# Kernel optimization log

Hardware: AMD Instinct MI355X
Metric: run time of the kernel (lower is better)

The kernel has to match this reference:

```python
import jax, jax.numpy as jnp
import numpy as np

EPS_LN = 1e-5


def _ln(x, g, b):
    m = jnp.mean(x, axis=-1, keepdims=True)
    v = jnp.var(x, axis=-1, keepdims=True)
    return (x - m) * jax.lax.rsqrt(v + EPS_LN) * g + b


def setup_inputs() -> dict:
    B, T, D, DV, NV, DS = 8, 2048, 128, 32, 64, 16
    key = jax.random.key(0)
    ks = jax.random.split(key, 24)
    s = 0.02
    inp = {
        'x_head': jax.random.normal(ks[0], (B, T, D), jnp.float32),
        'gate': jax.random.uniform(ks[1], (B, T, 1), jnp.float32),
        'mask': jnp.zeros((1, T, T), jnp.float32),
        'node_bias_6d': jax.random.normal(ks[2], (6,), jnp.float32),
        'vertex_emb': jax.random.normal(ks[3], (NV, DV), jnp.float32),
        'adj_bias': jax.random.normal(ks[4], (NV, NV), jnp.float32),
        'spectral_emb': jax.random.normal(ks[5], (NV, DS), jnp.float32),
        'fractal_W_spec_weight': jax.random.normal(ks[6], (DV, DS), jnp.float32),
        # learned params (torch Linear weight is [out, in])
        'cn_g': jnp.ones((D,), jnp.float32), 'cn_b': jnp.zeros((D,), jnp.float32),
        'Wq': jax.random.normal(ks[7], (D, D), jnp.float32) * s,
        'Wk': jax.random.normal(ks[8], (D, D), jnp.float32) * s,
        'Wv': jax.random.normal(ks[9], (D, D), jnp.float32) * s,
        'bn_g': jnp.ones((D,), jnp.float32), 'bn_b': jnp.zeros((D,), jnp.float32),
        'Wg_w': jax.random.normal(ks[10], (6, D), jnp.float32) * s,
        'Wg_b': jnp.zeros((6,), jnp.float32),
        'g2v': jax.random.normal(ks[11], (DV, 6), jnp.float32) * s,
        'v2h': jax.random.normal(ks[12], (D, DV), jnp.float32) * s,
        'pc_w': jax.random.normal(ks[13], (D, 2 * D), jnp.float32) * s,
        'pc_b': jnp.zeros((D,), jnp.float32),
        'pn_g': jnp.ones((D,), jnp.float32), 'pn_b': jnp.zeros((D,), jnp.float32),
        'pu_w': jax.random.normal(ks[14], (2 * D, D), jnp.float32) * s,
        'pu_b': jnp.zeros((2 * D,), jnp.float32),
        'pd_w': jax.random.normal(ks[15], (D, 2 * D), jnp.float32) * s,
        'pd_b': jnp.zeros((D,), jnp.float32),
    }
    return inp


def reference(x_head, gate, mask, node_bias_6d, vertex_emb, adj_bias, spectral_emb,
              fractal_W_spec_weight, cn_g, cn_b, Wq, Wk, Wv, bn_g, bn_b, Wg_w, Wg_b,
              g2v, v2h, pc_w, pc_b, pn_g, pn_b, pu_w, pu_b, pd_w, pd_b):
    d_head = x_head.shape[-1]
    scale = jnp.asarray(np.sqrt(d_head), jnp.float32)

    # --- center: gated attention (scores in fp32) ---
    h = _ln(x_head, cn_g, cn_b)
    Q = (h @ Wq.T) * gate
    K = (h @ Wk.T) * gate
    V = h @ Wv.T
    scores = jnp.einsum('btd,bsd->bts', Q.astype(jnp.float32), K.astype(jnp.float32)) / scale
    scores = scores + mask
    alignment = scores  # head_index == 0
    attn = jax.nn.softmax(scores, axis=-1).astype(x_head.dtype)
    center_out = jnp.einsum('bts,bsd->btd', attn, V)
    center_signal = x_head + center_out

    # --- boundary: hypercube vertex routing with top-8 straight-through ---
    h_b = _ln(x_head, bn_g, bn_b)
    gates_6d = jax.nn.sigmoid(h_b @ Wg_w.T + Wg_b + node_bias_6d)      # [B,T,6]
    gate_proj = gates_6d @ g2v.T                                       # [B,T,DV]
    v_scores = gate_proj @ vertex_emb.T                                # [B,T,NV]
    spec_proj = spectral_emb @ fractal_W_spec_weight.T                 # [NV,DV]
    v_scores = v_scores + 0.1 * (gate_proj @ spec_proj.T)
    v_scores = v_scores + 0.1 * (v_scores @ adj_bias)

    mean_abs = jax.lax.stop_gradient(jnp.maximum(jnp.mean(jnp.abs(v_scores)), 1e-6))
    v32 = (v_scores / mean_abs).astype(jnp.float32) * 3.0
    soft_pi = jax.nn.softmax(v32, axis=-1)                             # [B,T,NV]
    topk_vals, topk_idx = jax.lax.top_k(soft_pi, 8)                    # [B,T,8]
    nv = soft_pi.shape[-1]
    hard_pi = jnp.sum(jax.nn.one_hot(topk_idx, nv, dtype=soft_pi.dtype) * topk_vals[..., None], axis=-2)
    hard_pi = hard_pi / (jnp.sum(hard_pi, axis=-1, keepdims=True) + 1e-8)
    pi = (hard_pi - jax.lax.stop_gradient(soft_pi) + soft_pi).astype(x_head.dtype)

    vertex_ctx = pi @ vertex_emb                                       # [B,T,DV]
    boundary_signal = x_head + vertex_ctx @ v2h.T

    # --- field: gated FFN over combined signal ---
    phi_input = jnp.concatenate([center_signal, boundary_signal], axis=-1) @ pc_w.T + pc_b
    phi_h = _ln(phi_input, pn_g, pn_b)
    phi_out = jax.nn.gelu(phi_h @ pu_w.T + pu_b, approximate=False) @ pd_w.T + pd_b
    field_output = phi_input + phi_out
    return (field_output, pi, alignment)
```

## Files before the change

### kernel.cpp

```cpp
#include <hip/hip_runtime.h>
#include <cmath>

typedef __bf16 bf16_t;
typedef bf16_t bf16x8 __attribute__((ext_vector_type(8)));
typedef bf16_t bf16x4 __attribute__((ext_vector_type(4)));
typedef float f32x4 __attribute__((ext_vector_type(4)));

#define DEVI static __device__ __forceinline__

constexpr int TB = 8;
constexpr int TT = 2048;
constexpr int BT_ = TB * TT;
constexpr float EPS_LN = 1e-5f;

DEVI f32x4 mfma16(bf16x8 a, bf16x8 b, f32x4 c) {
  return __builtin_amdgcn_mfma_f32_16x16x32_bf16(a, b, c, 0, 0, 0);
}

DEVI bf16x8 cvt8(float4 a, float4 b) {
  bf16x8 v;
  v[0] = (bf16_t)a.x; v[1] = (bf16_t)a.y; v[2] = (bf16_t)a.z; v[3] = (bf16_t)a.w;
  v[4] = (bf16_t)b.x; v[5] = (bf16_t)b.y; v[6] = (bf16_t)b.z; v[7] = (bf16_t)b.w;
  return v;
}

DEVI void gload_lds16(const void* g, void* l) {
  __builtin_amdgcn_global_load_lds(
      (const __attribute__((address_space(1))) unsigned int*)g,
      (__attribute__((address_space(3))) unsigned int*)l, 16, 0, 0);
}

__global__ __launch_bounds__(256) void k_prep(
    const float* __restrict__ Wq, const float* __restrict__ Wk,
    const float* __restrict__ Wv, const float* __restrict__ Wpc,
    const float* __restrict__ Wpu, const float* __restrict__ Wpd,
    bf16_t* __restrict__ wf) {
  int g = blockIdx.x * 256 + threadIdx.x;
  const float* W;
  bf16_t* dst;
  int rel, lks, Kdim;
  if (g < 6144) {
    int m = g >> 11; rel = g & 2047;
    W = (m == 0) ? Wq : ((m == 1) ? Wk : Wv);
    dst = wf + m * 16384; lks = 2; Kdim = 128;
  } else if (g < 10240) {
    rel = g - 6144; W = Wpc; dst = wf + 49152; lks = 3; Kdim = 256;
  } else if (g < 14336) {
    rel = g - 10240; W = Wpu; dst = wf + 81920; lks = 2; Kdim = 128;
  } else {
    rel = g - 14336; W = Wpd; dst = wf + 114688; lks = 3; Kdim = 256;
  }
  int lane = rel & 63;
  int fk = (rel >> 6) & ((1 << lks) - 1);
  int n0 = rel >> (6 + lks);
  int row = n0 * 16 + (lane & 15);
  int col = fk * 32 + (lane >> 4) * 8;
  const float* s = W + row * Kdim + col;
  float4 a = *(const float4*)s;
  float4 b = *(const float4*)(s + 4);
  *(bf16x8*)(dst + (size_t)rel * 8) = cvt8(a, b);
}

__global__ __launch_bounds__(256) void k_qkv(
    const float* __restrict__ x, const float* __restrict__ gate,
    const float* __restrict__ cn_g, const float* __restrict__ cn_b,
    const bf16_t* __restrict__ wf,
    bf16_t* __restrict__ Qo, bf16_t* __restrict__ Ko, bf16_t* __restrict__ Vt) {
  __shared__ __align__(16) bf16_t sH[64 * 128];
  const int tid = threadIdx.x;
  const int t0 = blockIdx.x * 64;

  {
    const int tok = tid >> 2, part = tid & 3;
    const float* xr = x + (size_t)(t0 + tok) * 128 + part * 32;
    float v[32];
    float s0 = 0.f, s1 = 0.f;
#pragma unroll
    for (int i = 0; i < 8; ++i) {
      float4 f = ((const float4*)xr)[i];
      v[i * 4 + 0] = f.x; v[i * 4 + 1] = f.y; v[i * 4 + 2] = f.z; v[i * 4 + 3] = f.w;
      s0 += f.x + f.y + f.z + f.w;
      s1 += f.x * f.x + f.y * f.y + f.z * f.z + f.w * f.w;
    }
    s0 += __shfl_xor(s0, 1); s0 += __shfl_xor(s0, 2);
    s1 += __shfl_xor(s1, 1); s1 += __shfl_xor(s1, 2);
    float mean = s0 * (1.f / 128.f);
    float var = s1 * (1.f / 128.f) - mean * mean;
    float rstd = rsqrtf(var + EPS_LN);
#pragma unroll
    for (int j8 = 0; j8 < 4; ++j8) {
      bf16x8 hv;
#pragma unroll
      for (int k = 0; k < 8; ++k) {
        int d = part * 32 + j8 * 8 + k;
        float hn = (v[j8 * 8 + k] - mean) * rstd;
        hv[k] = (bf16_t)(hn * cn_g[d] + cn_b[d]);
      }
      int bl = part * 4 + j8;
      *(bf16x8*)(&sH[tok * 128 + ((bl ^ (tok & 7)) * 8)]) = hv;
    }
  }
  __syncthreads();

  const int wave = tid >> 6, lane = tid & 63;
  const int rt = lane & 15, kg = lane >> 4;
  const int arow = wave * 16 + rt;
  bf16x8 af[4];
#pragma unroll
  for (int ks = 0; ks < 4; ++ks)
    af[ks] = *(const bf16x8*)(&sH[arow * 128 + (((ks * 4 + kg) ^ (rt & 7)) * 8)]);

  const int trow0 = t0 + wave * 16 + kg * 4;
  float4 g4 = *(const float4*)(gate + trow0);
  float gr[4] = {g4.x, g4.y, g4.z, g4.w};
  const int b_ = trow0 >> 11;
  const int tloc = trow0 & 2047;

#pragma unroll
  for (int m = 0; m < 3; ++m) {
    const bf16_t* wm = wf + m * 16384;
#pragma unroll
    for (int n0 = 0; n0 < 8; ++n0) {
      f32x4 acc = {0.f, 0.f, 0.f, 0.f};
#pragma unroll
      for (int ks = 0; ks < 4; ++ks) {
        bf16x8 bf = *(const bf16x8*)(wm + ((size_t)(n0 * 4 + ks) * 64 + lane) * 8);
        acc = mfma16(af[ks], bf, acc);
      }
      if (m == 2) {
        bf16x4 pk;
        pk[0] = (bf16_t)acc[0]; pk[1] = (bf16_t)acc[1];
        pk[2] = (bf16_t)acc[2]; pk[3] = (bf16_t)acc[3];
        *(bf16x4*)(Vt + ((size_t)(b_ * 128 + n0 * 16 + rt)) * 2048 + tloc) = pk;
      } else {
        bf16_t* O = (m == 0) ? Qo : Ko;
#pragma unroll
        for (int r = 0; r < 4; ++r)
          O[(size_t)(trow0 + r) * 128 + n0 * 16 + rt] = (bf16_t)(acc[r] * gr[r]);
      }
    }
  }
}

__global__ __launch_bounds__(256) void k_vscores(
    const float* __restrict__ x, const float* __restrict__ bn_g,
    const float* __restrict__ bn_b, const float* __restrict__ Wg_w,
    const float* __restrict__ Wg_b, const float* __restrict__ nb6,
    const float* __restrict__ g2v, const float* __restrict__ vemb,
    const float* __restrict__ adj, const float* __restrict__ spec,
    const float* __restrict__ wspec,
    float* __restrict__ vs_out, float* __restrict__ psum) {
  __shared__ float sWg[768];
  __shared__ float sG2V[192];
  __shared__ float sVE[64 * 33];
  __shared__ float sSP[64 * 33];
  __shared__ float sADJ[64 * 64];
  __shared__ float sRaw[64 * 68];
  __shared__ float sBN[256];
  __shared__ float bsum;
  const int tid = threadIdx.x;
  const int t0 = blockIdx.x * 64;
  if (tid == 0) bsum = 0.f;
  for (int i = tid; i < 768; i += 256) sWg[i] = Wg_w[i];
  for (int i = tid; i < 192; i += 256) sG2V[i] = g2v[i];
  for (int i = tid; i < 256; i += 256) sBN[i] = (i < 128) ? bn_g[i] : bn_b[i - 128];
  for (int i = tid; i < 2048; i += 256) sVE[(i >> 5) * 33 + (i & 31)] = vemb[i];
  for (int i = tid; i < 4096; i += 256) sADJ[i] = adj[i];
  for (int i = tid; i < 2048; i += 256) {
    int s = i >> 5, vv = i & 31;
    float acc = 0.f;
#pragma unroll
    for (int e = 0; e < 16; ++e) acc += spec[s * 16 + e] * wspec[vv * 16 + e];
    sSP[s * 33 + vv] = acc;
  }
  __syncthreads();

  const int tok = tid >> 2, part = tid & 3;
  const float* xr = x + (size_t)(t0 + tok) * 128 + part * 32;
  float v[32];
  float s0 = 0.f, s1 = 0.f;
#pragma unroll
  for (int i = 0; i < 8; ++i) {
    float4 f = ((const float4*)xr)[i];
    v[i * 4 + 0] = f.x; v[i * 4 + 1] = f.y; v[i * 4 + 2] = f.z; v[i * 4 + 3] = f.w;
    s0 += f.x + f.y + f.z + f.w;
    s1 += f.x * f.x + f.y * f.y + f.z * f.z + f.w * f.w;
  }
  s0 += __shfl_xor(s0, 1); s0 += __shfl_xor(s0, 2);
  s1 += __shfl_xor(s1, 1); s1 += __shfl_xor(s1, 2);
  float mean = s0 * (1.f / 128.f);
  float rstd = rsqrtf(s1 * (1.f / 128.f) - mean * mean + EPS_LN);
  float hb[32];
#pragma unroll
  for (int k = 0; k < 32; ++k) {
    int d = part * 32 + k;
    hb[k] = (v[k] - mean) * rstd * sBN[d] + sBN[128 + d];
  }
  float g6[6];
#pragma unroll
  for (int j = 0; j < 6; ++j) {
    float a = 0.f;
#pragma unroll
    for (int k = 0; k < 32; ++k) a += hb[k] * sWg[j * 128 + part * 32 + k];
    a += __shfl_xor(a, 1); a += __shfl_xor(a, 2);
    a += Wg_b[j] + nb6[j];
    g6[j] = 1.f / (1.f + expf(-a));
  }
  float gp[32];
#pragma unroll
  for (int vv = 0; vv < 32; ++vv) {
    float a = 0.f;
#pragma unroll
    for (int j = 0; j < 6; ++j) a += g6[j] * sG2V[vv * 6 + j];
    gp[vv] = a;
  }
#pragma unroll
  for (int j = 0; j < 16; ++j) {
    int s = part * 16 + j;
    float a = 0.f;
#pragma unroll
    for (int vv = 0; vv < 32; ++vv)
      a += gp[vv] * (sVE[s * 33 + vv] + 0.1f * sSP[s * 33 + vv]);
    sRaw[tok * 68 + s] = a;
  }
  __syncthreads();

  float fin[16];
#pragma unroll
  for (int j = 0; j < 16; ++j) fin[j] = 0.f;
  for (int s = 0; s < 64; ++s) {
    float rv = sRaw[tok * 68 + s];
#pragma unroll
    for (int j = 0; j < 16; ++j) fin[j] += rv * sADJ[s * 64 + part * 16 + j];
  }
  float sa = 0.f;
#pragma unroll
  for (int j = 0; j < 16; ++j) {
    fin[j] = sRaw[tok * 68 + part * 16 + j] + 0.1f * fin[j];
    sa += fabsf(fin[j]);
  }
  float* o = vs_out + (size_t)(t0 + tok) * 64 + part * 16;
#pragma unroll
  for (int j4 = 0; j4 < 4; ++j4) {
    float4 f;
    f.x = fin[j4 * 4 + 0]; f.y = fin[j4 * 4 + 1];
    f.z = fin[j4 * 4 + 2]; f.w = fin[j4 * 4 + 3];
    ((float4*)o)[j4] = f;
  }
#pragma unroll
  for (int m = 1; m <= 32; m <<= 1) sa += __shfl_xor(sa, m);
  if ((tid & 63) == 0) atomicAdd(&bsum, sa);
  __syncthreads();
  if (tid == 0) psum[blockIdx.x] = bsum;
}

__global__ __launch_bounds__(256) void k_attn(
    const bf16_t* __restrict__ Q, const bf16_t* __restrict__ Kp,
    const bf16_t* __restrict__ Vt, const float* __restrict__ x,
    const float* __restrict__ mask,
    float* __restrict__ align_out, bf16_t* __restrict__ center) {
  __shared__ __align__(16) bf16_t sK[64 * 128];
  __shared__ __align__(16) bf16_t sV[128 * 64];
  __shared__ __align__(16) bf16_t sP[4][16 * 72];
  const int tid = threadIdx.x;
  const int b_ = blockIdx.x & 7;
  const int qt = blockIdx.x >> 3;
  const int wave = tid >> 6, lane = tid & 63;
  const int rt = lane & 15, kg = lane >> 4;
  const size_t tq0 = (size_t)b_ * TT + qt * 64;

  bf16x8 qf[4];
#pragma unroll
  for (int ks = 0; ks < 4; ++ks)
    qf[ks] = *(const bf16x8*)(Q + (tq0 + wave * 16 + rt) * 128 + ks * 32 + kg * 8);

  f32x4 o[8];
  f32x4 zero4 = {0.f, 0.f, 0.f, 0.f};
#pragma unroll
  for (int i = 0; i < 8; ++i) o[i] = zero4;
  float m[4], l[4];
#pragma unroll
  for (int r = 0; r < 4; ++r) { m[r] = -INFINITY; l[r] = 0.f; }
  const float inv_sc = 0.08838834764831845f;
  const int tqr = qt * 64 + wave * 16 + kg * 4;
  const int koff = wave * 1024 + lane * 16;

  for (int st = 0; st < 32; ++st) {
    const int sb = st * 64;
    __syncthreads();
#pragma unroll
    for (int i = 0; i < 4; ++i) {
      int off = i * 4096 + koff;
      int row = off >> 8;
      int c16 = (off >> 4) & 15;
      const char* src = (const char*)Kp +
          ((size_t)(b_ * TT + sb + row) * 128 + ((c16 ^ (row & 7)) * 8)) * 2;
      gload_lds16(src, (char*)sK + i * 4096 + wave * 1024);
    }
#pragma unroll
    for (int i = 0; i < 4; ++i) {
      int off = i * 4096 + koff;
      int row = off >> 7;
      int c16 = (off >> 4) & 7;
      const char* src = (const char*)Vt +
          ((size_t)(b_ * 128 + row) * 2048 + sb + ((c16 ^ (row & 7)) * 8)) * 2;
      gload_lds16(src, (char*)sV + i * 4096 + wave * 1024);
    }
    __syncthreads();

    float p[4][4];
#pragma unroll
    for (int ct = 0; ct < 4; ++ct) {
      const int brow = ct * 16 + rt;
      f32x4 acc = zero4;
#pragma unroll
      for (int ks = 0; ks < 4; ++ks) {
        bf16x8 kf = *(const bf16x8*)(&sK[brow * 128 + (((ks * 4 + kg) ^ (rt & 7)) * 8)]);
        acc = mfma16(qf[ks], kf, acc);
      }
      const int scol = sb + ct * 16 + rt;
#pragma unroll
      for (int r = 0; r < 4; ++r) {
        float sv = acc[r] * inv_sc + mask[(size_t)(tqr + r) * TT + scol];
        align_out[((size_t)b_ * TT + tqr + r) * TT + scol] = sv;
        p[ct][r] = sv;
      }
    }
    float mn[4], fsc[4];
#pragma unroll
    for (int r = 0; r < 4; ++r) {
      float pm = fmaxf(fmaxf(p[0][r], p[1][r]), fmaxf(p[2][r], p[3][r]));
#pragma unroll
      for (int dm = 1; dm <= 8; dm <<= 1) pm = fmaxf(pm, __shfl_xor(pm, dm));
      mn[r] = fmaxf(m[r], pm);
      fsc[r] = __expf(m[r] - mn[r]);
      m[r] = mn[r];
    }
    float rs[4] = {0.f, 0.f, 0.f, 0.f};
#pragma unroll
    for (int ct = 0; ct < 4; ++ct)
#pragma unroll
      for (int r = 0; r < 4; ++r) {
        float pe = __expf(p[ct][r] - mn[r]);
        p[ct][r] = pe;
        rs[r] += pe;
      }
#pragma unroll
    for (int r = 0; r < 4; ++r) {
#pragma unroll
      for (int dm = 1; dm <= 8; dm <<= 1) rs[r] += __shfl_xor(rs[r], dm);
      l[r] = l[r] * fsc[r] + rs[r];
    }
#pragma unroll
    for (int i = 0; i < 8; ++i) {
      o[i][0] *= fsc[0]; o[i][1] *= fsc[1]; o[i][2] *= fsc[2]; o[i][3] *= fsc[3];
    }
#pragma unroll
    for (int ct = 0; ct < 4; ++ct)
#pragma unroll
      for (int r = 0; r < 4; ++r)
        sP[wave][(kg * 4 + r) * 72 + ct * 16 + rt] = (bf16_t)p[ct][r];
    asm volatile("" ::: "memory");
    bf16x8 pf[2];
#pragma unroll
    for (int ks = 0; ks < 2; ++ks)
      pf[ks] = *(const bf16x8*)(&sP[wave][rt * 72 + ks * 32 + kg * 8]);
#pragma unroll
    for (int n0 = 0; n0 < 8; ++n0) {
      const int brow = n0 * 16 + rt;
      f32x4 acc = o[n0];
#pragma unroll
      for (int ks = 0; ks < 2; ++ks) {
        bf16x8 vf = *(const bf16x8*)(&sV[brow * 64 + (((ks * 4 + kg) ^ (rt & 7)) * 8)]);
        acc = mfma16(pf[ks], vf, acc);
      }
      o[n0] = acc;
    }
  }
  float il[4];
#pragma unroll
  for (int r = 0; r < 4; ++r) il[r] = 1.f / l[r];
  const size_t trow = tq0 + wave * 16 + kg * 4;
#pragma unroll
  for (int n0 = 0; n0 < 8; ++n0) {
    int col = n0 * 16 + rt;
#pragma unroll
    for (int r = 0; r < 4; ++r) {
      float val = o[n0][r] * il[r] + x[(trow + r) * 128 + col];
      center[(trow + r) * 128 + col] = (bf16_t)val;
    }
  }
}

__global__ __launch_bounds__(256) void k_pi(
    const float* __restrict__ x, const float* __restrict__ vs,
    const float* __restrict__ psum, const float* __restrict__ vemb,
    const float* __restrict__ v2h,
    float* __restrict__ pi_out, bf16_t* __restrict__ bound) {
  __shared__ float red[256];
  __shared__ float sVE[64 * 33];
  __shared__ float sV2H[128 * 33];
  const int tid = threadIdx.x;
  const int t0 = blockIdx.x * 64;
  red[tid] = psum[tid];
  for (int i = tid; i < 2048; i += 256) sVE[(i >> 5) * 33 + (i & 31)] = vemb[i];
  for (int i = tid; i < 4096; i += 256) sV2H[(i >> 5) * 33 + (i & 31)] = v2h[i];
  __syncthreads();
#pragma unroll
  for (int s = 128; s > 0; s >>= 1) {
    if (tid < s) red[tid] += red[tid + s];
    __syncthreads();
  }
  float mean_abs = fmaxf(red[0] * (1.f / 1048576.f), 1e-6f);
  float s3 = 3.f / mean_abs;

  const int tok = tid >> 2, part = tid & 3;
  const int tg = t0 + tok;
  const float* vr = vs + (size_t)tg * 64 + part * 16;
  float lg[16];
  float mx = -INFINITY;
#pragma unroll
  for (int j4 = 0; j4 < 4; ++j4) {
    float4 f = ((const float4*)vr)[j4];
    lg[j4 * 4 + 0] = f.x * s3; lg[j4 * 4 + 1] = f.y * s3;
    lg[j4 * 4 + 2] = f.z * s3; lg[j4 * 4 + 3] = f.w * s3;
    mx = fmaxf(mx, fmaxf(fmaxf(lg[j4 * 4 + 0], lg[j4 * 4 + 1]),
                         fmaxf(lg[j4 * 4 + 2], lg[j4 * 4 + 3])));
  }
  mx = fmaxf(mx, __shfl_xor(mx, 1));
  mx = fmaxf(mx, __shfl_xor(mx, 2));
  float e[16];
  float tot = 0.f;
#pragma unroll
  for (int j = 0; j < 16; ++j) { e[j] = expf(lg[j] - mx); tot += e[j]; }
  tot += __shfl_xor(tot, 1); tot += __shfl_xor(tot, 2);

  unsigned used = 0u;
  float tsum = 0.f;
#pragma unroll
  for (int it = 0; it < 8; ++it) {
    float bv = -INFINITY;
    int bi = 0;
#pragma unroll
    for (int j = 0; j < 16; ++j) {
      bool ok = !(used & (1u << j)) && (e[j] > bv);
      bv = ok ? e[j] : bv;
      bi = ok ? j : bi;
    }
    int gi = part * 16 + bi;
#pragma unroll
    for (int dm = 1; dm <= 2; dm <<= 1) {
      float ov = __shfl_xor(bv, dm);
      int oi = __shfl_xor(gi, dm);
      bool take = (ov > bv) || (ov == bv && oi < gi);
      bv = take ? ov : bv;
      gi = take ? oi : gi;
    }
    tsum += bv;
    if ((gi >> 4) == part) used |= 1u << (gi & 15);
  }
  float inv_tot = 1.f / tot;
  float inv_d = 1.f / (tsum * inv_tot + 1e-8f);
  float pi[16];
#pragma unroll
  for (int j = 0; j < 16; ++j)
    pi[j] = (used & (1u << j)) ? e[j] * inv_tot * inv_d : 0.f;
  float* po = pi_out + (size_t)tg * 64 + part * 16;
#pragma unroll
  for (int j4 = 0; j4 < 4; ++j4) {
    float4 f;
    f.x = pi[j4 * 4 + 0]; f.y = pi[j4 * 4 + 1];
    f.z = pi[j4 * 4 + 2]; f.w = pi[j4 * 4 + 3];
    ((float4*)po)[j4] = f;
  }
  float vc[32];
#pragma unroll
  for (int vv = 0; vv < 32; ++vv) vc[vv] = 0.f;
#pragma unroll
  for (int j = 0; j < 16; ++j) {
    float p = pi[j];
    int s = part * 16 + j;
#pragma unroll
    for (int vv = 0; vv < 32; ++vv) vc[vv] += p * sVE[s * 33 + vv];
  }
#pragma unroll
  for (int vv = 0; vv < 32; ++vv) {
    vc[vv] += __shfl_xor(vc[vv], 1);
    vc[vv] += __shfl_xor(vc[vv], 2);
  }
  const float* xr = x + (size_t)tg * 128 + part * 32;
  bf16_t* br = bound + (size_t)tg * 128 + part * 32;
#pragma unroll
  for (int d8 = 0; d8 < 4; ++d8) {
    float4 xa = ((const float4*)xr)[d8 * 2];
    float4 xb = ((const float4*)xr)[d8 * 2 + 1];
    float xv[8] = {xa.x, xa.y, xa.z, xa.w, xb.x, xb.y, xb.z, xb.w};
    bf16x8 ov;
#pragma unroll
    for (int k = 0; k < 8; ++k) {
      int d = part * 32 + d8 * 8 + k;
      float a = 0.f;
#pragma unroll
      for (int vv = 0; vv < 32; ++vv) a += vc[vv] * sV2H[d * 33 + vv];
      ov[k] = (bf16_t)(xv[k] + a);
    }
    *(bf16x8*)(br + d8 * 8) = ov;
  }
}

__global__ __launch_bounds__(256) void k_ffn(
    const bf16_t* __restrict__ center, const bf16_t* __restrict__ bound,
    const bf16_t* __restrict__ wf,
    const float* __restrict__ pc_b, const float* __restrict__ pn_g,
    const float* __restrict__ pn_b, const float* __restrict__ pu_b,
    const float* __restrict__ pd_b, float* __restrict__ out) {
  __shared__ __align__(16) bf16_t sH[64 * 128];
  __shared__ __align__(16) bf16_t sG[64 * 256];
  const bf16_t* wpc = wf + 49152;
  const bf16_t* wpu = wf + 81920;
  const bf16_t* wpd = wf + 114688;
  const int tid = threadIdx.x;
  const int t0 = blockIdx.x * 64;
  const int wave = tid >> 6, lane = tid & 63;
  const int rt = lane & 15, kg = lane >> 4;
  const int arow = wave * 16 + rt;

  bf16x8 af[8];
#pragma unroll
  for (int ks = 0; ks < 8; ++ks) {
    const bf16_t* src = (ks < 4)
        ? (center + (size_t)(t0 + arow) * 128 + ks * 32 + kg * 8)
        : (bound + (size_t)(t0 + arow) * 128 + (ks - 4) * 32 + kg * 8);
    af[ks] = *(const bf16x8*)src;
  }
  f32x4 phi[8];
#pragma unroll
  for (int n0 = 0; n0 < 8; ++n0) {
    f32x4 acc = {0.f, 0.f, 0.f, 0.f};
#pragma unroll
    for (int ks = 0; ks < 8; ++ks) {
      bf16x8 bf = *(const bf16x8*)(wpc + ((size_t)(n0 * 8 + ks) * 64 + lane) * 8);
      acc = mfma16(af[ks], bf, acc);
    }
    float bias = pc_b[n0 * 16 + rt];
    acc[0] += bias; acc[1] += bias; acc[2] += bias; acc[3] += bias;
    phi[n0] = acc;
  }
  float mean[4], rstd[4];
#pragma unroll
  for (int r = 0; r < 4; ++r) {
    float s0 = 0.f, s1 = 0.f;
#pragma unroll
    for (int n0 = 0; n0 < 8; ++n0) {
      float vv = phi[n0][r];
      s0 += vv; s1 += vv * vv;
    }
#pragma unroll
    for (int dm = 1; dm <= 8; dm <<= 1) {
      s0 += __shfl_xor(s0, dm);
      s1 += __shfl_xor(s1, dm);
    }
    mean[r] = s0 * (1.f / 128.f);
    float var = s1 * (1.f / 128.f) - mean[r] * mean[r];
    rstd[r] = rsqrtf(var + EPS_LN);
  }
#pragma unroll
  for (int n0 = 0; n0 < 8; ++n0) {
    int col = n0 * 16 + rt;
    float g = pn_g[col], bb = pn_b[col];
#pragma unroll
    for (int r = 0; r < 4; ++r) {
      float hv = (phi[n0][r] - mean[r]) * rstd[r] * g + bb;
      int row = wave * 16 + kg * 4 + r;
      *(bf16_t*)((char*)sH + row * 256 + ((2 * col) ^ ((row & 7) << 4))) = (bf16_t)hv;
    }
  }
  __syncthreads();

  bf16x8 ah[4];
#pragma unroll
  for (int ks = 0; ks < 4; ++ks)
    ah[ks] = *(const bf16x8*)((const char*)sH + arow * 256 +
                              (((ks * 4 + kg) ^ (rt & 7)) * 16));
#pragma unroll
  for (int half = 0; half < 2; ++half) {
#pragma unroll
    for (int n0h = 0; n0h < 8; ++n0h) {
      int n0 = half * 8 + n0h;
      f32x4 acc = {0.f, 0.f, 0.f, 0.f};
#pragma unroll
      for (int ks = 0; ks < 4; ++ks) {
        bf16x8 bf = *(const bf16x8*)(wpu + ((size_t)(n0 * 4 + ks) * 64 + lane) * 8);
        acc = mfma16(ah[ks], bf, acc);
      }
      int col = n0 * 16 + rt;
      float bias = pu_b[col];
#pragma unroll
      for (int r = 0; r < 4; ++r) {
        float uv = acc[r] + bias;
        float gv = 0.5f * uv * (1.f + erff(uv * 0.7071067811865476f));
        int row = wave * 16 + kg * 4 + r;
        *(bf16_t*)((char*)sG + row * 512 + ((2 * col) ^ ((row & 7) << 4))) = (bf16_t)gv;
      }
    }
  }
  __syncthreads();

  bf16x8 ag[8];
#pragma unroll
  for (int ks = 0; ks < 8; ++ks)
    ag[ks] = *(const bf16x8*)((const char*)sG + arow * 512 +
                              (((ks * 4 + kg) ^ (rt & 7)) * 16));
#pragma unroll
  for (int n0 = 0; n0 < 8; ++n0) {
    f32x4 acc = {0.f, 0.f, 0.f, 0.f};
#pragma unroll
    for (int ks = 0; ks < 8; ++ks) {
      bf16x8 bf = *(const bf16x8*)(wpd + ((size_t)(n0 * 8 + ks) * 64 + lane) * 8);
      acc = mfma16(ag[ks], bf, acc);
    }
    float bias = pd_b[n0 * 16 + rt];
#pragma unroll
    for (int r = 0; r < 4; ++r) {
      int row = wave * 16 + kg * 4 + r;
      out[(size_t)(t0 + row) * 128 + n0 * 16 + rt] = acc[r] + bias + phi[n0][r];
    }
  }
}

extern "C" void kernel_launch(void* const* d_in, const int* in_sizes, int n_in,
                              void* d_out, int out_size, void* d_ws, size_t ws_size,
                              hipStream_t stream) {
  (void)in_sizes; (void)n_in; (void)out_size; (void)ws_size;
  const float* x     = (const float*)d_in[0];
  const float* gate  = (const float*)d_in[1];
  const float* mask  = (const float*)d_in[2];
  const float* nb6   = (const float*)d_in[3];
  const float* vemb  = (const float*)d_in[4];
  const float* adj   = (const float*)d_in[5];
  const float* spec  = (const float*)d_in[6];
  const float* wspec = (const float*)d_in[7];
  const float* cn_g  = (const float*)d_in[8];
  const float* cn_b  = (const float*)d_in[9];
  const float* Wq    = (const float*)d_in[10];
  const float* Wk    = (const float*)d_in[11];
  const float* Wv    = (const float*)d_in[12];
  const float* bn_g  = (const float*)d_in[13];
  const float* bn_b  = (const float*)d_in[14];
  const float* Wg_w  = (const float*)d_in[15];
  const float* Wg_b  = (const float*)d_in[16];
  const float* g2v   = (const float*)d_in[17];
  const float* v2h   = (const float*)d_in[18];
  const float* pc_w  = (const float*)d_in[19];
  const float* pc_b  = (const float*)d_in[20];
  const float* pn_g  = (const float*)d_in[21];
  const float* pn_b  = (const float*)d_in[22];
  const float* pu_w  = (const float*)d_in[23];
  const float* pu_b  = (const float*)d_in[24];
  const float* pd_w  = (const float*)d_in[25];
  const float* pd_b  = (const float*)d_in[26];

  char* ws = (char*)d_ws;
  bf16_t* Qb   = (bf16_t*)(ws);
  bf16_t* Kb   = (bf16_t*)(ws + (4u << 20));
  bf16_t* Vt   = (bf16_t*)(ws + (8u << 20));
  bf16_t* bnd  = (bf16_t*)(ws + (12u << 20));
  bf16_t* ctr  = (bf16_t*)(ws + (16u << 20));
  float*  vsc  = (float*)(ws + (20u << 20));
  float*  psum = (float*)(ws + (24u << 20));
  bf16_t* wfb  = (bf16_t*)(ws + (24u << 20) + 4096);

  float* f_out = (float*)d_out;
  float* pi_o  = f_out + (size_t)BT_ * 128;
  float* al_o  = pi_o + (size_t)BT_ * 64;

  k_prep<<<72, 256, 0, stream>>>(Wq, Wk, Wv, pc_w, pu_w, pd_w, wfb);
  k_qkv<<<256, 256, 0, stream>>>(x, gate, cn_g, cn_b, wfb, Qb, Kb, Vt);
  k_vscores<<<256, 256, 0, stream>>>(x, bn_g, bn_b, Wg_w, Wg_b, nb6, g2v, vemb,
                                     adj, spec, wspec, vsc, psum);
  k_attn<<<256, 256, 0, stream>>>(Qb, Kb, Vt, x, mask, al_o, ctr);
  k_pi<<<256, 256, 0, stream>>>(x, vsc, psum, vemb, v2h, pi_o, bnd);
  k_ffn<<<256, 256, 0, stream>>>(ctr, bnd, wfb, pc_b, pn_g, pn_b, pu_b, pd_b, f_out);
}
```

Baseline: 386.4 us.

## Split attention over keys, double-buffer K/V, and widen grids of qkv and ffn

Attention is split across two key-range halves (flash-decoding style) with partial outputs and m/l statistics combined in a new k_comb kernel, and K/V tiles are double-buffered in LDS so the next load overlaps compute. The qkv and ffn kernels now launch 512 blocks, splitting output columns across blocks or waves to fill more CUs on a 256-CU part. expf is swapped for __expf in two places. The split adds an extra kernel and fp32 partial-output traffic, and its path depends on the workspace size.

```diff
diff --git a/kernel.cpp b/kernel.cpp
--- a/kernel.cpp
+++ b/kernel.cpp
@@ -68,7 +68,8 @@
     bf16_t* __restrict__ Qo, bf16_t* __restrict__ Ko, bf16_t* __restrict__ Vt) {
   __shared__ __align__(16) bf16_t sH[64 * 128];
   const int tid = threadIdx.x;
-  const int t0 = blockIdx.x * 64;
+  const int sel = blockIdx.x >> 8;
+  const int t0 = (blockIdx.x & 255) * 64;
 
   {
     const int tok = tid >> 2, part = tid & 3;
@@ -116,9 +117,9 @@
   const int b_ = trow0 >> 11;
   const int tloc = trow0 & 2047;
 
-#pragma unroll
-  for (int m = 0; m < 3; ++m) {
-    const bf16_t* wm = wf + m * 16384;
+  {
+    const bf16_t* wm = wf + sel * 16384;
+    bf16_t* O = sel ? Ko : Qo;
 #pragma unroll
     for (int n0 = 0; n0 < 8; ++n0) {
       f32x4 acc = {0.f, 0.f, 0.f, 0.f};
@@ -127,17 +128,26 @@
         bf16x8 bf = *(const bf16x8*)(wm + ((size_t)(n0 * 4 + ks) * 64 + lane) * 8);
         acc = mfma16(af[ks], bf, acc);
       }
-      if (m == 2) {
-        bf16x4 pk;
-        pk[0] = (bf16_t)acc[0]; pk[1] = (bf16_t)acc[1];
-        pk[2] = (bf16_t)acc[2]; pk[3] = (bf16_t)acc[3];
-        *(bf16x4*)(Vt + ((size_t)(b_ * 128 + n0 * 16 + rt)) * 2048 + tloc) = pk;
-      } else {
-        bf16_t* O = (m == 0) ? Qo : Ko;
-#pragma unroll
-        for (int r = 0; r < 4; ++r)
-          O[(size_t)(trow0 + r) * 128 + n0 * 16 + rt] = (bf16_t)(acc[r] * gr[r]);
-      }
+#pragma unroll
+      for (int r = 0; r < 4; ++r)
+        O[(size_t)(trow0 + r) * 128 + n0 * 16 + rt] = (bf16_t)(acc[r] * gr[r]);
+    }
+  }
+  {
+    const bf16_t* wv = wf + 2 * 16384;
+#pragma unroll
+    for (int n0h = 0; n0h < 4; ++n0h) {
+      int n0 = sel * 4 + n0h;
+      f32x4 acc = {0.f, 0.f, 0.f, 0.f};
+#pragma unroll
+      for (int ks = 0; ks < 4; ++ks) {
+        bf16x8 bf = *(const bf16x8*)(wv + ((size_t)(n0 * 4 + ks) * 64 + lane) * 8);
+        acc = mfma16(af[ks], bf, acc);
+      }
+      bf16x4 pk;
+      pk[0] = (bf16_t)acc[0]; pk[1] = (bf16_t)acc[1];
+      pk[2] = (bf16_t)acc[2]; pk[3] = (bf16_t)acc[3];
+      *(bf16x4*)(Vt + ((size_t)(b_ * 128 + n0 * 16 + rt)) * 2048 + tloc) = pk;
     }
   }
 }
@@ -204,7 +214,7 @@
     for (int k = 0; k < 32; ++k) a += hb[k] * sWg[j * 128 + part * 32 + k];
     a += __shfl_xor(a, 1); a += __shfl_xor(a, 2);
     a += Wg_b[j] + nb6[j];
-    g6[j] = 1.f / (1.f + expf(-a));
+    g6[j] = 1.f / (1.f + __expf(-a));
   }
   float gp[32];
 #pragma unroll
@@ -257,14 +267,18 @@
 __global__ __launch_bounds__(256) void k_attn(
     const bf16_t* __restrict__ Q, const bf16_t* __restrict__ Kp,
     const bf16_t* __restrict__ Vt, const float* __restrict__ x,
-    const float* __restrict__ mask,
-    float* __restrict__ align_out, bf16_t* __restrict__ center) {
-  __shared__ __align__(16) bf16_t sK[64 * 128];
-  __shared__ __align__(16) bf16_t sV[128 * 64];
+    const float* __restrict__ mask, float* __restrict__ align_out,
+    bf16_t* __restrict__ center, float* __restrict__ o_part,
+    float* __restrict__ ml_part, int nsplit) {
+  __shared__ __align__(16) bf16_t sK[2][64 * 128];
+  __shared__ __align__(16) bf16_t sV[2][128 * 64];
   __shared__ __align__(16) bf16_t sP[4][16 * 72];
   const int tid = threadIdx.x;
   const int b_ = blockIdx.x & 7;
-  const int qt = blockIdx.x >> 3;
+  const int qt = (blockIdx.x >> 3) & 31;
+  const int sq = blockIdx.x >> 8;
+  const int ntile = 32 / nsplit;
+  const int st0 = sq * ntile;
   const int wave = tid >> 6, lane = tid & 63;
   const int rt = lane & 15, kg = lane >> 4;
   const size_t tq0 = (size_t)b_ * TT + qt * 64;
@@ -285,17 +299,16 @@
   const int tqr = qt * 64 + wave * 16 + kg * 4;
   const int koff = wave * 1024 + lane * 16;
 
-  for (int st = 0; st < 32; ++st) {
-    const int sb = st * 64;
-    __syncthreads();
+  auto stage = [&](int buf, int st) {
+    const int sb2 = st * 64;
 #pragma unroll
     for (int i = 0; i < 4; ++i) {
       int off = i * 4096 + koff;
       int row = off >> 8;
       int c16 = (off >> 4) & 15;
       const char* src = (const char*)Kp +
-          ((size_t)(b_ * TT + sb + row) * 128 + ((c16 ^ (row & 7)) * 8)) * 2;
-      gload_lds16(src, (char*)sK + i * 4096 + wave * 1024);
+          ((size_t)(b_ * TT + sb2 + row) * 128 + ((c16 ^ (row & 7)) * 8)) * 2;
+      gload_lds16(src, (char*)(&sK[buf][0]) + i * 4096 + wave * 1024);
     }
 #pragma unroll
     for (int i = 0; i < 4; ++i) {
@@ -303,10 +316,17 @@
       int row = off >> 7;
       int c16 = (off >> 4) & 7;
       const char* src = (const char*)Vt +
-          ((size_t)(b_ * 128 + row) * 2048 + sb + ((c16 ^ (row & 7)) * 8)) * 2;
-      gload_lds16(src, (char*)sV + i * 4096 + wave * 1024);
-    }
+          ((size_t)(b_ * 128 + row) * 2048 + sb2 + ((c16 ^ (row & 7)) * 8)) * 2;
+      gload_lds16(src, (char*)(&sV[buf][0]) + i * 4096 + wave * 1024);
+    }
+  };
+
+  int cur = 0;
+  stage(0, st0);
+  for (int it = 0; it < ntile; ++it) {
+    const int sb = (st0 + it) * 64;
     __syncthreads();
+    if (it + 1 < ntile) stage(cur ^ 1, st0 + it + 1);
 
     float p[4][4];
 #pragma unroll
@@ -315,7 +335,7 @@
       f32x4 acc = zero4;
 #pragma unroll
       for (int ks = 0; ks < 4; ++ks) {
-        bf16x8 kf = *(const bf16x8*)(&sK[brow * 128 + (((ks * 4 + kg) ^ (rt & 7)) * 8)]);
+        bf16x8 kf = *(const bf16x8*)(&sK[cur][brow * 128 + (((ks * 4 + kg) ^ (rt & 7)) * 8)]);
         acc = mfma16(qf[ks], kf, acc);
       }
       const int scol = sb + ct * 16 + rt;
@@ -371,24 +391,83 @@
       f32x4 acc = o[n0];
 #pragma unroll
       for (int ks = 0; ks < 2; ++ks) {
-        bf16x8 vf = *(const bf16x8*)(&sV[brow * 64 + (((ks * 4 + kg) ^ (rt & 7)) * 8)]);
+        bf16x8 vf = *(const bf16x8*)(&sV[cur][brow * 64 + (((ks * 4 + kg) ^ (rt & 7)) * 8)]);
         acc = mfma16(pf[ks], vf, acc);
       }
       o[n0] = acc;
     }
-  }
-  float il[4];
-#pragma unroll
-  for (int r = 0; r < 4; ++r) il[r] = 1.f / l[r];
+    cur ^= 1;
+  }
+
   const size_t trow = tq0 + wave * 16 + kg * 4;
-#pragma unroll
-  for (int n0 = 0; n0 < 8; ++n0) {
-    int col = n0 * 16 + rt;
-#pragma unroll
-    for (int r = 0; r < 4; ++r) {
-      float val = o[n0][r] * il[r] + x[(trow + r) * 128 + col];
-      center[(trow + r) * 128 + col] = (bf16_t)val;
-    }
+  if (nsplit == 1) {
+    float il[4];
+#pragma unroll
+    for (int r = 0; r < 4; ++r) il[r] = 1.f / l[r];
+#pragma unroll
+    for (int n0 = 0; n0 < 8; ++n0) {
+      int col = n0 * 16 + rt;
+#pragma unroll
+      for (int r = 0; r < 4; ++r) {
+        float val = o[n0][r] * il[r] + x[(trow + r) * 128 + col];
+        center[(trow + r) * 128 + col] = (bf16_t)val;
+      }
+    }
+  } else {
+#pragma unroll
+    for (int n0 = 0; n0 < 8; ++n0) {
+      int col = n0 * 16 + rt;
+#pragma unroll
+      for (int r = 0; r < 4; ++r)
+        o_part[((size_t)sq * BT_ + trow + r) * 128 + col] = o[n0][r];
+    }
+    if (rt == 0) {
+#pragma unroll
+      for (int r = 0; r < 4; ++r) {
+        size_t t = (size_t)sq * BT_ + trow + r;
+        ml_part[t * 2] = m[r];
+        ml_part[t * 2 + 1] = l[r];
+      }
+    }
+  }
+}
+
+__global__ __launch_bounds__(256) void k_comb(
+    const float* __restrict__ x, const float* __restrict__ o_part,
+    const float* __restrict__ ml_part, bf16_t* __restrict__ center) {
+  const int tid = threadIdx.x;
+  const int tok = blockIdx.x * 64 + (tid >> 2);
+  const int part = tid & 3;
+  float m0 = ml_part[(size_t)tok * 2];
+  float l0 = ml_part[(size_t)tok * 2 + 1];
+  float m1 = ml_part[((size_t)BT_ + tok) * 2];
+  float l1 = ml_part[((size_t)BT_ + tok) * 2 + 1];
+  float M = fmaxf(m0, m1);
+  float w0 = __expf(m0 - M), w1 = __expf(m1 - M);
+  float inv = 1.f / (l0 * w0 + l1 * w1);
+  w0 *= inv; w1 *= inv;
+  const float* xr = x + (size_t)tok * 128 + part * 32;
+  const float* o0 = o_part + (size_t)tok * 128 + part * 32;
+  const float* o1 = o_part + ((size_t)BT_ + tok) * 128 + part * 32;
+  bf16_t* cr = center + (size_t)tok * 128 + part * 32;
+#pragma unroll
+  for (int c = 0; c < 4; ++c) {
+    float4 a0 = ((const float4*)(o0 + c * 8))[0];
+    float4 b0 = ((const float4*)(o0 + c * 8))[1];
+    float4 a1 = ((const float4*)(o1 + c * 8))[0];
+    float4 b1 = ((const float4*)(o1 + c * 8))[1];
+    float4 xa = ((const float4*)(xr + c * 8))[0];
+    float4 xb = ((const float4*)(xr + c * 8))[1];
+    bf16x8 ov;
+    ov[0] = (bf16_t)(a0.x * w0 + a1.x * w1 + xa.x);
+    ov[1] = (bf16_t)(a0.y * w0 + a1.y * w1 + xa.y);
+    ov[2] = (bf16_t)(a0.z * w0 + a1.z * w1 + xa.z);
+    ov[3] = (bf16_t)(a0.w * w0 + a1.w * w1 + xa.w);
+    ov[4] = (bf16_t)(b0.x * w0 + b1.x * w1 + xb.x);
+    ov[5] = (bf16_t)(b0.y * w0 + b1.y * w1 + xb.y);
+    ov[6] = (bf16_t)(b0.z * w0 + b1.z * w1 + xb.z);
+    ov[7] = (bf16_t)(b0.w * w0 + b1.w * w1 + xb.w);
+    *(bf16x8*)(cr + c * 8) = ov;
   }
 }
 
@@ -432,7 +511,7 @@
   float e[16];
   float tot = 0.f;
 #pragma unroll
-  for (int j = 0; j < 16; ++j) { e[j] = expf(lg[j] - mx); tot += e[j]; }
+  for (int j = 0; j < 16; ++j) { e[j] = __expf(lg[j] - mx); tot += e[j]; }
   tot += __shfl_xor(tot, 1); tot += __shfl_xor(tot, 2);
 
   unsigned used = 0u;
@@ -514,16 +593,18 @@
     const float* __restrict__ pc_b, const float* __restrict__ pn_g,
     const float* __restrict__ pn_b, const float* __restrict__ pu_b,
     const float* __restrict__ pd_b, float* __restrict__ out) {
-  __shared__ __align__(16) bf16_t sH[64 * 128];
-  __shared__ __align__(16) bf16_t sG[64 * 256];
+  __shared__ __align__(16) bf16_t sH[32 * 128];
+  __shared__ __align__(16) bf16_t sG[32 * 256];
+  __shared__ float sLN[2][32][2];
   const bf16_t* wpc = wf + 49152;
   const bf16_t* wpu = wf + 81920;
   const bf16_t* wpd = wf + 114688;
   const int tid = threadIdx.x;
-  const int t0 = blockIdx.x * 64;
+  const int t0 = blockIdx.x * 32;
   const int wave = tid >> 6, lane = tid & 63;
+  const int g = wave & 1, h = wave >> 1;
   const int rt = lane & 15, kg = lane >> 4;
-  const int arow = wave * 16 + rt;
+  const int arow = g * 16 + rt;
 
   bf16x8 af[8];
 #pragma unroll
@@ -533,9 +614,10 @@
         : (bound + (size_t)(t0 + arow) * 128 + (ks - 4) * 32 + kg * 8);
     af[ks] = *(const bf16x8*)src;
   }
-  f32x4 phi[8];
-#pragma unroll
-  for (int n0 = 0; n0 < 8; ++n0) {
+  f32x4 phi[4];
+#pragma unroll
+  for (int j = 0; j < 4; ++j) {
+    int n0 = 4 * h + j;
     f32x4 acc = {0.f, 0.f, 0.f, 0.f};
 #pragma unroll
     for (int ks = 0; ks < 8; ++ks) {
@@ -544,15 +626,14 @@
     }
     float bias = pc_b[n0 * 16 + rt];
     acc[0] += bias; acc[1] += bias; acc[2] += bias; acc[3] += bias;
-    phi[n0] = acc;
-  }
-  float mean[4], rstd[4];
+    phi[j] = acc;
+  }
 #pragma unroll
   for (int r = 0; r < 4; ++r) {
     float s0 = 0.f, s1 = 0.f;
 #pragma unroll
-    for (int n0 = 0; n0 < 8; ++n0) {
-      float vv = phi[n0][r];
+    for (int j = 0; j < 4; ++j) {
+      float vv = phi[j][r];
       s0 += vv; s1 += vv * vv;
     }
 #pragma unroll
@@ -560,18 +641,31 @@
       s0 += __shfl_xor(s0, dm);
       s1 += __shfl_xor(s1, dm);
     }
+    if (rt == 0) {
+      int row = g * 16 + kg * 4 + r;
+      sLN[h][row][0] = s0;
+      sLN[h][row][1] = s1;
+    }
+  }
+  __syncthreads();
+  float mean[4], rstd[4];
+#pragma unroll
+  for (int r = 0; r < 4; ++r) {
+    int row = g * 16 + kg * 4 + r;
+    float s0 = sLN[0][row][0] + sLN[1][row][0];
+    float s1 = sLN[0][row][1] + sLN[1][row][1];
     mean[r] = s0 * (1.f / 128.f);
     float var = s1 * (1.f / 128.f) - mean[r] * mean[r];
     rstd[r] = rsqrtf(var + EPS_LN);
   }
 #pragma unroll
-  for (int n0 = 0; n0 < 8; ++n0) {
-    int col = n0 * 16 + rt;
-    float g = pn_g[col], bb = pn_b[col];
+  for (int j = 0; j < 4; ++j) {
+    int col = (4 * h + j) * 16 + rt;
+    float gg = pn_g[col], bb = pn_b[col];
 #pragma unroll
     for (int r = 0; r < 4; ++r) {
-      float hv = (phi[n0][r] - mean[r]) * rstd[r] * g + bb;
-      int row = wave * 16 + kg * 4 + r;
+      float hv = (phi[j][r] - mean[r]) * rstd[r] * gg + bb;
+      int row = g * 16 + kg * 4 + r;
       *(bf16_t*)((char*)sH + row * 256 + ((2 * col) ^ ((row & 7) << 4))) = (bf16_t)hv;
     }
   }
@@ -583,25 +677,22 @@
     ah[ks] = *(const bf16x8*)((const char*)sH + arow * 256 +
                               (((ks * 4 + kg) ^ (rt & 7)) * 16));
 #pragma unroll
-  for (int half = 0; half < 2; ++half) {
-#pragma unroll
-    for (int n0h = 0; n0h < 8; ++n0h) {
-      int n0 = half * 8 + n0h;
-      f32x4 acc = {0.f, 0.f, 0.f, 0.f};
-#pragma unroll
-      for (int ks = 0; ks < 4; ++ks) {
-        bf16x8 bf = *(const bf16x8*)(wpu + ((size_t)(n0 * 4 + ks) * 64 + lane) * 8);
-        acc = mfma16(ah[ks], bf, acc);
-      }
-      int col = n0 * 16 + rt;
-      float bias = pu_b[col];
-#pragma unroll
-      for (int r = 0; r < 4; ++r) {
-        float uv = acc[r] + bias;
-        float gv = 0.5f * uv * (1.f + erff(uv * 0.7071067811865476f));
-        int row = wave * 16 + kg * 4 + r;
-        *(bf16_t*)((char*)sG + row * 512 + ((2 * col) ^ ((row & 7) << 4))) = (bf16_t)gv;
-      }
+  for (int j2 = 0; j2 < 8; ++j2) {
+    int n0 = 8 * h + j2;
+    f32x4 acc = {0.f, 0.f, 0.f, 0.f};
+#pragma unroll
+    for (int ks = 0; ks < 4; ++ks) {
+      bf16x8 bf = *(const bf16x8*)(wpu + ((size_t)(n0 * 4 + ks) * 64 + lane) * 8);
+      acc = mfma16(ah[ks], bf, acc);
+    }
+    int col = n0 * 16 + rt;
+    float bias = pu_b[col];
+#pragma unroll
+    for (int r = 0; r < 4; ++r) {
+      float uv = acc[r] + bias;
+      float gv = 0.5f * uv * (1.f + erff(uv * 0.7071067811865476f));
+      int row = g * 16 + kg * 4 + r;
+      *(bf16_t*)((char*)sG + row * 512 + ((2 * col) ^ ((row & 7) << 4))) = (bf16_t)gv;
     }
   }
   __syncthreads();
@@ -612,7 +703,8 @@
     ag[ks] = *(const bf16x8*)((const char*)sG + arow * 512 +
                               (((ks * 4 + kg) ^ (rt & 7)) * 16));
 #pragma unroll
-  for (int n0 = 0; n0 < 8; ++n0) {
+  for (int j = 0; j < 4; ++j) {
+    int n0 = 4 * h + j;
     f32x4 acc = {0.f, 0.f, 0.f, 0.f};
 #pragma unroll
     for (int ks = 0; ks < 8; ++ks) {
@@ -622,8 +714,8 @@
     float bias = pd_b[n0 * 16 + rt];
 #pragma unroll
     for (int r = 0; r < 4; ++r) {
-      int row = wave * 16 + kg * 4 + r;
-      out[(size_t)(t0 + row) * 128 + n0 * 16 + rt] = acc[r] + bias + phi[n0][r];
+      int row = g * 16 + kg * 4 + r;
+      out[(size_t)(t0 + row) * 128 + n0 * 16 + rt] = acc[r] + bias + phi[j][r];
     }
   }
 }
@@ -631,7 +723,7 @@
 extern "C" void kernel_launch(void* const* d_in, const int* in_sizes, int n_in,
                               void* d_out, int out_size, void* d_ws, size_t ws_size,
                               hipStream_t stream) {
-  (void)in_sizes; (void)n_in; (void)out_size; (void)ws_size;
+  (void)in_sizes; (void)n_in; (void)out_size;
   const float* x     = (const float*)d_in[0];
   const float* gate  = (const float*)d_in[1];
   const float* mask  = (const float*)d_in[2];
@@ -669,16 +761,23 @@
   float*  vsc  = (float*)(ws + (20u << 20));
   float*  psum = (float*)(ws + (24u << 20));
   bf16_t* wfb  = (bf16_t*)(ws + (24u << 20) + 4096);
+  float*  mlp  = (float*)(ws + (24u << 20) + (512u << 10));
+  float*  opart= (float*)(ws + (25u << 20));
+
+  const int nsplit = (ws_size >= ((size_t)41 << 20) + 65536) ? 2 : 1;
 
   float* f_out = (float*)d_out;
   float* pi_o  = f_out + (size_t)BT_ * 128;
   float* al_o  = pi_o + (size_t)BT_ * 64;
 
   k_prep<<<72, 256, 0, stream>>>(Wq, Wk, Wv, pc_w, pu_w, pd_w, wfb);
-  k_qkv<<<256, 256, 0, stream>>>(x, gate, cn_g, cn_b, wfb, Qb, Kb, Vt);
+  k_qkv<<<512, 256, 0, stream>>>(x, gate, cn_g, cn_b, wfb, Qb, Kb, Vt);
   k_vscores<<<256, 256, 0, stream>>>(x, bn_g, bn_b, Wg_w, Wg_b, nb6, g2v, vemb,
                                      adj, spec, wspec, vsc, psum);
-  k_attn<<<256, 256, 0, stream>>>(Qb, Kb, Vt, x, mask, al_o, ctr);
+  k_attn<<<256 * nsplit, 256, 0, stream>>>(Qb, Kb, Vt, x, mask, al_o, ctr,
+                                           opart, mlp, nsplit);
+  if (nsplit == 2)
+    k_comb<<<256, 256, 0, stream>>>(x, opart, mlp, ctr);
   k_pi<<<256, 256, 0, stream>>>(x, vsc, psum, vemb, v2h, pi_o, bnd);
-  k_ffn<<<256, 256, 0, stream>>>(ctr, bnd, wfb, pc_b, pn_g, pn_b, pu_b, pd_b, f_out);
-}
+  k_ffn<<<512, 256, 0, stream>>>(ctr, bnd, wfb, pc_b, pn_g, pn_b, pu_b, pd_b, f_out);
+}
```

Result: faster. 360.8 us (-6.6%).
